# Kernel tuning notes

Hardware: AMD Instinct MI355X
Metric: run time of the kernel (lower is better)

The kernel has to match this reference:

```python
import jax, jax.numpy as jnp
import numpy as np

DIM = 1024
HEADS = 16
HEAD_DIM = DIM // HEADS
SCALE = HEAD_DIM ** -0.5


def setup_inputs() -> dict:
    key = jax.random.key(0)
    k1, k2, k3, k4 = jax.random.split(key, 4)
    x = jax.random.normal(k1, (4, 2048, DIM), dtype=jnp.float32)
    # nn.Linear weights stored as [out, in]; qkv_bias=False so no proj_in bias
    w_qkv = jax.random.normal(k2, (3 * DIM, DIM), dtype=jnp.float32) * (DIM ** -0.5)
    w_out = jax.random.normal(k3, (DIM, DIM), dtype=jnp.float32) * (DIM ** -0.5)
    b_out = jax.random.normal(k4, (DIM,), dtype=jnp.float32) * 0.01
    return {"x": x, "w_qkv": w_qkv, "w_out": w_out, "b_out": b_out}


def reference(x, w_qkv, w_out, b_out):
    bs, ns, _ = x.shape
    qkv = jnp.einsum("bsd,ed->bse", x, w_qkv)              # [b, s, 3*dim]
    qkv = qkv.reshape(bs, ns, 3, HEADS, HEAD_DIM)
    qkv = jnp.transpose(qkv, (2, 0, 3, 1, 4))               # [3, b, h, s, hd]
    q, k, v = qkv[0], qkv[1], qkv[2]
    attn = jnp.einsum("bhqd,bhkd->bhqk", q, k) * SCALE      # [b, h, s, s]
    attn = jax.nn.softmax(attn, axis=-1)
    out = jnp.einsum("bhqk,bhkd->bhqd", attn, v)            # [b, h, s, hd]
    out = jnp.transpose(out, (0, 2, 1, 3)).reshape(bs, ns, HEADS * HEAD_DIM)
    return jnp.einsum("bsd,ed->bse", out, w_out) + b_out
```

## Files before the change

kernel.cpp:

```cpp
#include <hip/hip_runtime.h>

#define DIM 1024
#define SEQ 2048

typedef unsigned short ushort_t;
typedef unsigned int u32;
typedef __attribute__((ext_vector_type(8))) short short8;
typedef __attribute__((ext_vector_type(8))) unsigned short ushort8;
typedef __attribute__((ext_vector_type(4))) float f32x4;
typedef __attribute__((ext_vector_type(16))) float f32x16;

__device__ __forceinline__ ushort_t f2bf(float x) {
    u32 u = __float_as_uint(x);
    u32 r = (u + 0x7fffu + ((u >> 16) & 1u)) >> 16;
    return (ushort_t)r;
}

__device__ __forceinline__ u32 cvtpk(float lo, float hi) {
    u32 r;
    asm("v_cvt_pk_bf16_f32 %0, %1, %2" : "=v"(r) : "v"(lo), "v"(hi));
    return r;
}

__device__ __forceinline__ void gload16(const void* g, void* l) {
    __builtin_amdgcn_global_load_lds(
        (const __attribute__((address_space(1))) u32*)g,
        (__attribute__((address_space(3))) u32*)l, 16, 0, 0);
}

__device__ __forceinline__ int swz8(int row, int col) {
    return row * 64 + ((((col >> 3) ^ (row & 7)) << 3) | (col & 7));
}

__global__ __launch_bounds__(256) void cvt_bf16(const float* __restrict__ in,
                                                ushort_t* __restrict__ out, int n8) {
    for (int i = blockIdx.x * blockDim.x + threadIdx.x; i < n8; i += gridDim.x * blockDim.x) {
        const float4 a = ((const float4*)in)[2 * i];
        const float4 b = ((const float4*)in)[2 * i + 1];
        ushort8 o;
        o[0] = f2bf(a.x); o[1] = f2bf(a.y); o[2] = f2bf(a.z); o[3] = f2bf(a.w);
        o[4] = f2bf(b.x); o[5] = f2bf(b.y); o[6] = f2bf(b.z); o[7] = f2bf(b.w);
        ((ushort8*)out)[i] = o;
    }
}

template <int EPI>
__global__ __launch_bounds__(256) void gemm_bt(const ushort_t* __restrict__ A,
                                               const ushort_t* __restrict__ B,
                                               const float* __restrict__ bias,
                                               ushort_t* __restrict__ outb,
                                               ushort_t* __restrict__ voutb,
                                               float* __restrict__ outf) {
    __shared__ __align__(16) ushort_t As[128 * 64];
    __shared__ __align__(16) ushort_t Bs[128 * 64];
    const int t = threadIdx.x;
    const int m0 = blockIdx.y * 128, n0 = blockIdx.x * 128;
    const int w = t >> 6, lane = t & 63, k15 = lane & 15, g = lane >> 4;
    const int wm = (w >> 1) * 64, wn = (w & 1) * 64;
    const int srow = t >> 3, scol = (t & 7) * 8;

    f32x4 acc[4][4] = {};

    for (int k0 = 0; k0 < 1024; k0 += 64) {
        __syncthreads();
        #pragma unroll
        for (int i = 0; i < 4; ++i) {
            gload16(&A[(size_t)(m0 + i * 32 + srow) * 1024 + k0 + scol],
                    ((char*)As) + i * 4096 + t * 16);
            gload16(&B[(size_t)(n0 + i * 32 + srow) * 1024 + k0 + scol],
                    ((char*)Bs) + i * 4096 + t * 16);
        }
        __syncthreads();
        #pragma unroll
        for (int ks = 0; ks < 2; ++ks) {
            short8 af[4], bf[4];
            #pragma unroll
            for (int i = 0; i < 4; ++i) {
                af[i] = *(const short8*)&As[(wm + i * 16 + k15) * 64 + ks * 32 + g * 8];
                bf[i] = *(const short8*)&Bs[(wn + i * 16 + k15) * 64 + ks * 32 + g * 8];
            }
            #pragma unroll
            for (int mi = 0; mi < 4; ++mi)
                #pragma unroll
                for (int ni = 0; ni < 4; ++ni)
                    acc[mi][ni] = __builtin_amdgcn_mfma_f32_16x16x32_bf16(
                        af[mi], bf[ni], acc[mi][ni], 0, 0, 0);
        }
    }

    if (EPI == 0) {
        #pragma unroll
        for (int mi = 0; mi < 4; ++mi) {
            const int mbase = m0 + wm + mi * 16 + g * 4;
            const int b = mbase >> 11, s0 = mbase & 2047;
            #pragma unroll
            for (int ni = 0; ni < 4; ++ni) {
                const int e = n0 + wn + ni * 16 + k15;
                const int qi = e >> 10, h = (e >> 6) & 15, hd = e & 63;
                const int bh = b * 16 + h;
                if (qi == 2) {
                    const u32 lo = cvtpk(acc[mi][ni][0], acc[mi][ni][1]);
                    const u32 hi = cvtpk(acc[mi][ni][2], acc[mi][ni][3]);
                    *(uint2*)&voutb[((size_t)bh * 64 + hd) * SEQ + s0] = make_uint2(lo, hi);
                } else {
                    const float scl = (qi == 0) ? 0.180336880f : 1.0f;
                    #pragma unroll
                    for (int r = 0; r < 4; ++r)
                        outb[((size_t)(qi * 64 + bh) * SEQ + s0 + r) * 64 + hd] =
                            f2bf(acc[mi][ni][r] * scl);
                }
            }
        }
    } else {
        #pragma unroll
        for (int mi = 0; mi < 4; ++mi) {
            #pragma unroll
            for (int r = 0; r < 4; ++r) {
                const size_t m = m0 + wm + mi * 16 + g * 4 + r;
                #pragma unroll
                for (int ni = 0; ni < 4; ++ni) {
                    const int e = n0 + wn + ni * 16 + k15;
                    outf[m * 1024 + e] = acc[mi][ni][r] + bias[e];
                }
            }
        }
    }
}

__global__ __launch_bounds__(256, 2) void attn_mfma(const ushort_t* __restrict__ qk,
                                                    const ushort_t* __restrict__ vt,
                                                    ushort_t* __restrict__ aout) {
    __shared__ __align__(16) ushort_t Ks[2][64 * 64];
    __shared__ __align__(16) ushort_t Vs[2][64 * 64];

    const int t = threadIdx.x, w = t >> 6, lane = t & 63;
    const int l31 = lane & 31, hi = lane >> 5;

    const int bid = blockIdx.x;
    const int j   = bid >> 3;
    const int bh  = ((bid & 7) << 3) + (j >> 3);
    const int q0  = (j & 7) * 256;

    const ushort_t* Qp = qk + (size_t)bh * SEQ * 64;
    const ushort_t* Kp = qk + (size_t)(64 + bh) * SEQ * 64;
    const ushort_t* Vp = vt + (size_t)bh * 64 * SEQ;
    const int wqA = q0 + w * 64 + l31;
    const int wqB = wqA + 32;

    const int srow = t >> 3;
    const int scb8 = ((t & 7) ^ (srow & 7)) * 8;

    const ushort_t* kpA = Kp + (size_t)srow * 64 + scb8;
    const ushort_t* vpA = Vp + (size_t)srow * SEQ + scb8;

    short8 qfA[4], qfB[4];
    #pragma unroll
    for (int kc = 0; kc < 4; ++kc) {
        qfA[kc] = *(const short8*)&Qp[(size_t)wqA * 64 + kc * 16 + hi * 8];
        qfB[kc] = *(const short8*)&Qp[(size_t)wqB * 64 + kc * 16 + hi * 8];
    }

    gload16(kpA,            ((char*)Ks) + t * 16);
    gload16(kpA + 32 * 64,  ((char*)Ks) + 4096 + t * 16);
    gload16(vpA,            ((char*)Vs) + t * 16);
    gload16(vpA + 32 * SEQ, ((char*)Vs) + 4096 + t * 16);
    kpA += 64 * 64; vpA += 64;
    __syncthreads();

    f32x16 oA[2] = {}, oB[2] = {};
    float liA = 0.f, liB = 0.f;
    int cur = 0;

    for (int kt = 0; kt < SEQ / 64; ++kt) {
        if (kt + 1 < SEQ / 64) {
            char* dstK = ((char*)Ks) + (cur ^ 1) * 8192 + t * 16;
            char* dstV = ((char*)Vs) + (cur ^ 1) * 8192 + t * 16;
            gload16(kpA,            dstK);
            gload16(kpA + 32 * 64,  dstK + 4096);
            gload16(vpA,            dstV);
            gload16(vpA + 32 * SEQ, dstV + 4096);
            kpA += 64 * 64; vpA += 64;
        }

        f32x16 sA[2] = {}, sB[2] = {};
        __builtin_amdgcn_s_setprio(1);
        #pragma unroll
        for (int kt2 = 0; kt2 < 2; ++kt2) {
            #pragma unroll
            for (int kc = 0; kc < 4; ++kc) {
                const short8 kf = *(const short8*)&Ks[cur][swz8(kt2 * 32 + l31, kc * 16 + hi * 8)];
                sA[kt2] = __builtin_amdgcn_mfma_f32_32x32x16_bf16(kf, qfA[kc], sA[kt2], 0, 0, 0);
                sB[kt2] = __builtin_amdgcn_mfma_f32_32x32x16_bf16(kf, qfB[kc], sB[kt2], 0, 0, 0);
            }
        }
        __builtin_amdgcn_s_setprio(0);

        uint4 pbA[4], pbB[4];
        {
            float t0 = 0.f, t1 = 0.f, t2 = 0.f, t3 = 0.f;
            #pragma unroll
            for (int kt2 = 0; kt2 < 2; ++kt2)
                #pragma unroll
                for (int r = 0; r < 16; r += 4) {
                    const float e0 = __builtin_amdgcn_exp2f(sA[kt2][r + 0]);
                    const float e1 = __builtin_amdgcn_exp2f(sA[kt2][r + 1]);
                    const float e2 = __builtin_amdgcn_exp2f(sA[kt2][r + 2]);
                    const float e3 = __builtin_amdgcn_exp2f(sA[kt2][r + 3]);
                    sA[kt2][r + 0] = e0; sA[kt2][r + 1] = e1;
                    sA[kt2][r + 2] = e2; sA[kt2][r + 3] = e3;
                    t0 += e0; t1 += e1; t2 += e2; t3 += e3;
                }
            float rs = (t0 + t1) + (t2 + t3);
            rs += __shfl_xor(rs, 32);
            liA += rs;
            #pragma unroll
            for (int ks2 = 0; ks2 < 4; ++ks2) {
                const int r0 = (ks2 & 1) * 8;
                const int sv = ks2 >> 1;
                u32 pA = cvtpk(sA[sv][r0 + 0], sA[sv][r0 + 1]);
                u32 pB = cvtpk(sA[sv][r0 + 2], sA[sv][r0 + 3]);
                u32 pC = cvtpk(sA[sv][r0 + 4], sA[sv][r0 + 5]);
                u32 pD = cvtpk(sA[sv][r0 + 6], sA[sv][r0 + 7]);
                asm volatile("v_permlane32_swap_b32 %0, %1" : "+v"(pA), "+v"(pC));
                asm volatile("v_permlane32_swap_b32 %0, %1" : "+v"(pB), "+v"(pD));
                pbA[ks2] = make_uint4(pA, pB, pC, pD);
            }
        }
        {
            float t0 = 0.f, t1 = 0.f, t2 = 0.f, t3 = 0.f;
            #pragma unroll
            for (int kt2 = 0; kt2 < 2; ++kt2)
                #pragma unroll
                for (int r = 0; r < 16; r += 4) {
                    const float e0 = __builtin_amdgcn_exp2f(sB[kt2][r + 0]);
                    const float e1 = __builtin_amdgcn_exp2f(sB[kt2][r + 1]);
                    const float e2 = __builtin_amdgcn_exp2f(sB[kt2][r + 2]);
                    const float e3 = __builtin_amdgcn_exp2f(sB[kt2][r + 3]);
                    sB[kt2][r + 0] = e0; sB[kt2][r + 1] = e1;
                    sB[kt2][r + 2] = e2; sB[kt2][r + 3] = e3;
                    t0 += e0; t1 += e1; t2 += e2; t3 += e3;
                }
            float rs = (t0 + t1) + (t2 + t3);
            rs += __shfl_xor(rs, 32);
            liB += rs;
            #pragma unroll
            for (int ks2 = 0; ks2 < 4; ++ks2) {
                const int r0 = (ks2 & 1) * 8;
                const int sv = ks2 >> 1;
                u32 pA = cvtpk(sB[sv][r0 + 0], sB[sv][r0 + 1]);
                u32 pB = cvtpk(sB[sv][r0 + 2], sB[sv][r0 + 3]);
                u32 pC = cvtpk(sB[sv][r0 + 4], sB[sv][r0 + 5]);
                u32 pD = cvtpk(sB[sv][r0 + 6], sB[sv][r0 + 7]);
                asm volatile("v_permlane32_swap_b32 %0, %1" : "+v"(pA), "+v"(pC));
                asm volatile("v_permlane32_swap_b32 %0, %1" : "+v"(pB), "+v"(pD));
                pbB[ks2] = make_uint4(pA, pB, pC, pD);
            }
        }

        __builtin_amdgcn_s_setprio(1);
        #pragma unroll
        for (int dt = 0; dt < 2; ++dt) {
            #pragma unroll
            for (int ks2 = 0; ks2 < 4; ++ks2) {
                const short8 vf = *(const short8*)&Vs[cur][swz8(dt * 32 + l31, ks2 * 16 + hi * 8)];
                oA[dt] = __builtin_amdgcn_mfma_f32_32x32x16_bf16(
                    vf, *(const short8*)&pbA[ks2], oA[dt], 0, 0, 0);
                oB[dt] = __builtin_amdgcn_mfma_f32_32x32x16_bf16(
                    vf, *(const short8*)&pbB[ks2], oB[dt], 0, 0, 0);
            }
        }
        __builtin_amdgcn_s_setprio(0);

        __syncthreads();
        cur ^= 1;
    }

    const int b = bh >> 4, h = bh & 15;
    {
        const float inv = 1.0f / liA;
        const size_t base = ((size_t)b * SEQ + wqA) * DIM + h * 64;
        #pragma unroll
        for (int dt = 0; dt < 2; ++dt)
            #pragma unroll
            for (int rq = 0; rq < 4; ++rq) {
                const u32 lo = cvtpk(oA[dt][4 * rq + 0] * inv, oA[dt][4 * rq + 1] * inv);
                const u32 hg = cvtpk(oA[dt][4 * rq + 2] * inv, oA[dt][4 * rq + 3] * inv);
                *(uint2*)&aout[base + dt * 32 + rq * 8 + hi * 4] = make_uint2(lo, hg);
            }
    }
    {
        const float inv = 1.0f / liB;
        const size_t base = ((size_t)b * SEQ + wqB) * DIM + h * 64;
        #pragma unroll
        for (int dt = 0; dt < 2; ++dt)
            #pragma unroll
            for (int rq = 0; rq < 4; ++rq) {
                const u32 lo = cvtpk(oB[dt][4 * rq + 0] * inv, oB[dt][4 * rq + 1] * inv);
                const u32 hg = cvtpk(oB[dt][4 * rq + 2] * inv, oB[dt][4 * rq + 3] * inv);
                *(uint2*)&aout[base + dt * 32 + rq * 8 + hi * 4] = make_uint2(lo, hg);
            }
    }
}

extern "C" void kernel_launch(void* const* d_in, const int* in_sizes, int n_in,
                              void* d_out, int out_size, void* d_ws, size_t ws_size,
                              hipStream_t stream) {
    const float* x     = (const float*)d_in[0];
    const float* w_qkv = (const float*)d_in[1];
    const float* w_out = (const float*)d_in[2];
    const float* b_out = (const float*)d_in[3];
    float* out = (float*)d_out;

    char* ws = (char*)d_ws;
    ushort_t* xb    = (ushort_t*)ws;
    ushort_t* wqkvb = (ushort_t*)(ws + (size_t)16 * 1024 * 1024);
    ushort_t* woutb = (ushort_t*)(ws + (size_t)22 * 1024 * 1024);
    ushort_t* qkb   = (ushort_t*)(ws + (size_t)24 * 1024 * 1024);
    ushort_t* vtb   = (ushort_t*)(ws + (size_t)56 * 1024 * 1024);
    ushort_t* aob   = (ushort_t*)(ws + (size_t)72 * 1024 * 1024);

    cvt_bf16<<<1024, 256, 0, stream>>>(x,     xb,    8192 * 1024 / 8);
    cvt_bf16<<<512,  256, 0, stream>>>(w_qkv, wqkvb, 3072 * 1024 / 8);
    cvt_bf16<<<256,  256, 0, stream>>>(w_out, woutb, 1024 * 1024 / 8);

    gemm_bt<0><<<dim3(24, 64), 256, 0, stream>>>(xb, wqkvb, nullptr, qkb, vtb, nullptr);
    attn_mfma<<<512, 256, 0, stream>>>(qkb, vtb, aob);
    gemm_bt<1><<<dim3(8, 64), 256, 0, stream>>>(aob, woutb, b_out, nullptr, nullptr, out);
}
```

Before: 202.9 us.

## Merge bf16 conversions into one kernel and swizzle QKV GEMM block order

Replaces three separate fp32-to-bf16 conversion launches with a single grid-stride kernel covering x, w_qkv and w_out, which removes two launches and their tail gaps. Remaps QKV GEMM block indices so consecutive blocks are spread across XCD-sized groups to improve L2 locality. Adds a minimum-occupancy hint to the GEMM launch bounds. The remap and occupancy hint could also change cache behaviour or register allocation unfavourably.

```diff
diff --git a/kernel.cpp b/kernel.cpp
--- a/kernel.cpp
+++ b/kernel.cpp
@@ -32,29 +32,47 @@
     return row * 64 + ((((col >> 3) ^ (row & 7)) << 3) | (col & 7));
 }
 
-__global__ __launch_bounds__(256) void cvt_bf16(const float* __restrict__ in,
-                                                ushort_t* __restrict__ out, int n8) {
-    for (int i = blockIdx.x * blockDim.x + threadIdx.x; i < n8; i += gridDim.x * blockDim.x) {
-        const float4 a = ((const float4*)in)[2 * i];
-        const float4 b = ((const float4*)in)[2 * i + 1];
+__global__ __launch_bounds__(256) void cvt_all(const float* __restrict__ x,
+                                               const float* __restrict__ wq,
+                                               const float* __restrict__ wo,
+                                               ushort_t* __restrict__ xb,
+                                               ushort_t* __restrict__ wqb,
+                                               ushort_t* __restrict__ wob) {
+    for (int i = blockIdx.x * blockDim.x + threadIdx.x; i < 1572864;
+         i += gridDim.x * blockDim.x) {
+        const float* in; ushort_t* out; int off;
+        if (i < 1048576)      { in = x;  out = xb;  off = i; }
+        else if (i < 1441792) { in = wq; out = wqb; off = i - 1048576; }
+        else                  { in = wo; out = wob; off = i - 1441792; }
+        const float4 a = ((const float4*)in)[2 * off];
+        const float4 b = ((const float4*)in)[2 * off + 1];
         ushort8 o;
         o[0] = f2bf(a.x); o[1] = f2bf(a.y); o[2] = f2bf(a.z); o[3] = f2bf(a.w);
         o[4] = f2bf(b.x); o[5] = f2bf(b.y); o[6] = f2bf(b.z); o[7] = f2bf(b.w);
-        ((ushort8*)out)[i] = o;
+        ((ushort8*)out)[off] = o;
     }
 }
 
 template <int EPI>
-__global__ __launch_bounds__(256) void gemm_bt(const ushort_t* __restrict__ A,
-                                               const ushort_t* __restrict__ B,
-                                               const float* __restrict__ bias,
-                                               ushort_t* __restrict__ outb,
-                                               ushort_t* __restrict__ voutb,
-                                               float* __restrict__ outf) {
+__global__ __launch_bounds__(256, 5) void gemm_bt(const ushort_t* __restrict__ A,
+                                                  const ushort_t* __restrict__ B,
+                                                  const float* __restrict__ bias,
+                                                  ushort_t* __restrict__ outb,
+                                                  ushort_t* __restrict__ voutb,
+                                                  float* __restrict__ outf) {
     __shared__ __align__(16) ushort_t As[128 * 64];
     __shared__ __align__(16) ushort_t Bs[128 * 64];
     const int t = threadIdx.x;
-    const int m0 = blockIdx.y * 128, n0 = blockIdx.x * 128;
+
+    int bx = blockIdx.x, by = blockIdx.y;
+    if (EPI == 0) {
+        const int bid = bx + by * 24;
+        const int swzb = (bid & 7) * 192 + (bid >> 3);
+        bx = swzb % 24;
+        by = swzb / 24;
+    }
+    const int m0 = by * 128, n0 = bx * 128;
+
     const int w = t >> 6, lane = t & 63, k15 = lane & 15, g = lane >> 4;
     const int wm = (w >> 1) * 64, wn = (w & 1) * 64;
     const int srow = t >> 3, scol = (t & 7) * 8;
@@ -319,9 +337,7 @@
     ushort_t* vtb   = (ushort_t*)(ws + (size_t)56 * 1024 * 1024);
     ushort_t* aob   = (ushort_t*)(ws + (size_t)72 * 1024 * 1024);
 
-    cvt_bf16<<<1024, 256, 0, stream>>>(x,     xb,    8192 * 1024 / 8);
-    cvt_bf16<<<512,  256, 0, stream>>>(w_qkv, wqkvb, 3072 * 1024 / 8);
-    cvt_bf16<<<256,  256, 0, stream>>>(w_out, woutb, 1024 * 1024 / 8);
+    cvt_all<<<2048, 256, 0, stream>>>(x, w_qkv, w_out, xb, wqkvb, woutb);
 
     gemm_bt<0><<<dim3(24, 64), 256, 0, stream>>>(xb, wqkvb, nullptr, qkb, vtb, nullptr);
     attn_mfma<<<512, 256, 0, stream>>>(qkb, vtb, aob);
```

Measured after the change: 253.3 us. +24.8%, slower.
